# Kernel tuning notes

Measured on AMD Instinct MI355X. Metric: run time of the kernel, lower is better.

Reference implementation:

```python
import math
import jax, jax.numpy as jnp
import numpy as np

T_STEPS = 65536
T_S = 1.0      # net_params['t_s']
THETA = 10.0   # net_params['af_params']['theta']


def _eps_func(mult, tau, epsilon, t_end, t_s):
    vals = []
    for t in np.arange(0, t_end, t_s):
        v = mult * t / tau * math.exp(1 - t / tau)
        if abs(v) < abs(epsilon) and t > tau:
            break
        vals.append(v)
    return vals


def _srm_kernel(mult, tau, epsilon, t_end, t_s):
    # replicates SlayerTrainer._calculate_srm_kernel: pad-to-odd, prepend zeros, flip
    k = _eps_func(mult, tau, epsilon, t_end, t_s)
    if len(k) % 2 == 0:
        k.append(0.0)
    k = np.asarray(k, dtype=np.float32)
    k = np.concatenate([np.zeros(len(k) - 1, np.float32), k])[::-1].copy()
    return k  # (K,), K odd; causal after cross-correlation with pad K//2


def setup_inputs() -> dict:
    key = jax.random.key(0)
    k1, k2, k3 = jax.random.split(key, 3)
    x = jax.random.uniform(k1, (1, 1, 1, 250, T_STEPS), jnp.float32)
    srm = jnp.asarray(_srm_kernel(1.0, 10.0, 1e-4, 200, T_S))                 # sr_params
    ref = jnp.asarray(np.asarray(_eps_func(-20.0, 1.0, 1e-4, 200, T_S), np.float32))  # ref_params
    # SpikeLinear weights, init N(0, std=weights_init)
    w1 = jax.random.normal(k2, (25, 250), jnp.float32) * 4.0
    w2 = jax.random.normal(k3, (1, 25), jnp.float32) * 4.0
    return {"x": x, "srm": srm, "ref": ref, "w1": w1, "w2": w2}


def srm_conv(z, srm):
    # z: (C, T). Per-channel 1-D cross-correlation with 'same' padding,
    # equal to F.conv3d(x, eye-SRM kernel, padding=(0,0,K//2)) * t_s.
    K = srm.shape[0]
    p = K // 2
    lhs = z[:, None, :]            # (C, 1, T) -- channels as batch
    rhs = srm[None, None, :]       # (1, 1, K)
    out = jax.lax.conv_general_dilated(
        lhs, rhs, window_strides=(1,), padding=[(p, p)],
        dimension_numbers=("NCW", "OIW", "NCW"))
    return out[:, 0, :] * T_S


def gen_spikes(pot, ref):
    # Sequential integrate-fire with refractory feedback (slayer_cuda.get_spikes_cuda).
    # pot: (C, T). Carry = per-neuron buffer of scheduled future refractory additions.
    C = pot.shape[0]
    L = ref.shape[0]
    # ref[j] is added to potentials[t+j] on a spike at t (ref[0]==0); after the
    # shift, buf[0] corresponds to time t+1, so schedule ref[1:].
    ref_next = jnp.concatenate([ref[1:], jnp.zeros((1,), pot.dtype)])

    def step(buf, p_t):
        u = p_t + buf[:, 0]                           # membrane incl. refractory
        s = (u >= THETA).astype(pot.dtype)
        buf = jnp.concatenate([buf[:, 1:], jnp.zeros((C, 1), pot.dtype)], axis=1)
        buf = buf + s[:, None] * ref_next[None, :]
        return buf, (u, s / T_S)

    buf0 = jnp.zeros((C, L), pot.dtype)
    _, (u_seq, s_seq) = jax.lax.scan(step, buf0, pot.T)
    return u_seq.T, s_seq.T  # (C, T), (C, T)


def reference(x, srm, ref, w1, w2):
    h = srm_conv(x[0, 0, 0], srm)        # (250, T) SRM-filtered input spikes
    h = w1 @ h                           # (25, T)  SpikeLinear fc1
    _, s1 = gen_spikes(h, ref)           # (25, T)  spikes layer 1
    h = srm_conv(s1, srm)                # (25, T)  SRM on hidden spikes
    h = w2 @ h                           # (1, T)   SpikeLinear fc2
    _, s2 = gen_spikes(h, ref)           # (1, T)
    return s2.reshape(1, 1, 1, 1, -1)
```

## Files before the change

kernel.cpp:

```cpp
#include <hip/hip_runtime.h>


#define T_LEN   65536
#define NCH     250
#define NO1     25
#define KTAPS   129
#define PAD     128
#define SRM_LEN 257
#define REF_LEN 16
#define THETA_F 10.0f
#define LBLK    128
#define NBK     512
#define WARM    128
#define TS      256
#define TT      128
#define FTILE   1024
#define NWORDS  (T_LEN / 32)
#define NGRP    16

__device__ __forceinline__ void srm_step(float p, const float (&rn)[15], float (&b)[15],
                                         unsigned &m, float &sf_out) {
  float u = p + b[0];
  unsigned sp = (u >= THETA_F) ? 1u : 0u;
  float sf = sp ? 1.0f : 0.0f;
#pragma unroll
  for (int j = 0; j < 14; ++j) b[j] = __builtin_fmaf(sf, rn[j], b[j + 1]);
  b[14] = __fmul_rn(sf, rn[14]);
  m = (m << 1) | sp;
  sf_out = sf;
}

__global__ void k_fill(float* out, float v) {
  out[blockIdx.x * 256 + threadIdx.x] = v;
}

__global__ __launch_bounds__(256) void k_prep(const float* __restrict__ w1,
                                              float* __restrict__ w1T) {
  for (int i = threadIdx.x; i < NO1 * NCH; i += 256) {
    int c = i / NO1, o = i - c * NO1;
    w1T[i] = w1[o * NCH + c];
  }
}

__global__ __launch_bounds__(1024, 4) void k_mm1(const float* __restrict__ x,
                                                 const float* __restrict__ w1T,
                                                 float* __restrict__ y1t) {
  __shared__ __align__(16) float part[NGRP][5][TT];
  const int tid = threadIdx.x;
  const int lane = tid & 63;
  const int wv = __builtin_amdgcn_readfirstlane(tid >> 6);
  const int t0 = blockIdx.x * TT;
  const int cs = wv * 15 + (wv < 10 ? wv : 10);
  const int cn = (wv < 10) ? 16 : 15;
  float acc[NO1][2];
#pragma unroll
  for (int o = 0; o < NO1; ++o) { acc[o][0] = 0.f; acc[o][1] = 0.f; }
  const float* xp = x + (size_t)cs * T_LEN + t0 + lane * 2;
  const float* wt = w1T + cs * NO1;
  float2 xb0 = *(const float2*)xp;
  float2 xb1 = *(const float2*)(xp + T_LEN);
  for (int ci = 0; ci < cn; ++ci) {
    float2 xv = xb0;
    xb0 = xb1;
    xb1 = (ci + 2 < cn) ? *(const float2*)(xp + (size_t)(ci + 2) * T_LEN)
                        : make_float2(0.f, 0.f);
    const float* wr = wt + ci * NO1;
#pragma unroll
    for (int o = 0; o < NO1; ++o) {
      float wvv = wr[o];
      acc[o][0] = __builtin_fmaf(wvv, xv.x, acc[o][0]);
      acc[o][1] = __builtin_fmaf(wvv, xv.y, acc[o][1]);
    }
  }
  float* yb = y1t + (size_t)blockIdx.x * (NO1 * TT);
#pragma unroll
  for (int r = 0; r < 5; ++r) {
#pragma unroll
    for (int oo = 0; oo < 5; ++oo) {
      int o = r * 5 + oo;
      *(float2*)&part[wv][oo][lane * 2] = make_float2(acc[o][0], acc[o][1]);
    }
    __syncthreads();
    if (tid < 5 * (TT / 4)) {
      int oo = tid >> 5;
      int p4 = (tid & 31) * 4;
      float4 s = *(const float4*)&part[0][oo][p4];
#pragma unroll
      for (int g = 1; g < NGRP; ++g) {
        float4 p = *(const float4*)&part[g][oo][p4];
        s.x = __fadd_rn(s.x, p.x);
        s.y = __fadd_rn(s.y, p.y);
        s.z = __fadd_rn(s.z, p.z);
        s.w = __fadd_rn(s.w, p.w);
      }
      *(float4*)&yb[(r * 5 + oo) * TT + p4] = s;
    }
    __syncthreads();
  }
}

__global__ __launch_bounds__(256, 8) void k_fir1(const float* __restrict__ y1t,
                                                 const float* __restrict__ srm,
                                                 float* __restrict__ pot1) {
  __shared__ __align__(16) float win[FTILE + PAD];
  const int tid = threadIdx.x;
  const int o = blockIdx.y;
  const int t0 = blockIdx.x * FTILE;
  for (int j = tid; j < FTILE + PAD; j += 256) {
    int g = t0 - PAD + j;
    win[j] = (g >= 0)
        ? y1t[(size_t)(g >> 7) * (NO1 * TT) + o * TT + (g & (TT - 1))] : 0.0f;
  }
  __syncthreads();
  const int base = tid * 4;
  float q0 = 0.0f, q1 = 0.0f, q2 = 0.0f, q3 = 0.0f;
#pragma unroll
  for (int i = 32; i >= 0; --i) {
    float4 v = *(const float4*)&win[base + 4 * i];
#pragma unroll
    for (int l = 3; l >= 0; --l) {
      float vl = (l == 0) ? v.x : (l == 1) ? v.y : (l == 2) ? v.z : v.w;
#pragma unroll
      for (int k = 0; k < 4; ++k) {
        int d = 128 + k - 4 * i - l;
        if (d >= 0 && d <= 128) {
          float e = srm[4 * i + l - k];
          if (k == 0) q0 = __builtin_fmaf(e, vl, q0);
          else if (k == 1) q1 = __builtin_fmaf(e, vl, q1);
          else if (k == 2) q2 = __builtin_fmaf(e, vl, q2);
          else q3 = __builtin_fmaf(e, vl, q3);
        }
      }
    }
  }
  *(float4*)&pot1[(size_t)o * T_LEN + t0 + base] = make_float4(q0, q1, q2, q3);
}

__global__ __launch_bounds__(TS) void k_pot2(const unsigned* __restrict__ s1p,
                                             const float* __restrict__ srm,
                                             const float* __restrict__ w2,
                                             float* __restrict__ pot2) {
  __shared__ float zs[TS + PAD];
  const int tid = threadIdx.x;
  const int t0 = blockIdx.x * TS;
  const int g0 = t0 - PAD;
  {
    int g = g0 + tid;
    float z = 0.0f;
    if (g >= 0) {
      int wi = g >> 5, sh = g & 31;
#pragma unroll
      for (int o = 0; o < NO1; ++o) {
        unsigned wvv = s1p[o * NWORDS + wi];
        z += ((wvv >> sh) & 1u) ? w2[o] : 0.0f;
      }
    }
    zs[tid] = z;
    if (tid < PAD) {
      int g2 = g0 + TS + tid;
      int wi = g2 >> 5, sh = g2 & 31;
      float z2 = 0.0f;
#pragma unroll
      for (int o = 0; o < NO1; ++o) {
        unsigned wvv = s1p[o * NWORDS + wi];
        z2 += ((wvv >> sh) & 1u) ? w2[o] : 0.0f;
      }
      zs[TS + tid] = z2;
    }
  }
  __syncthreads();
  float a = 0.0f;
#pragma unroll
  for (int d = 0; d < KTAPS; ++d) {
    float e = srm[PAD - d];
    a = __builtin_fmaf(e, zs[PAD + tid - d], a);
  }
  pot2[t0 + tid] = a;
}

template <int C, bool PACKED>
__global__ __launch_bounds__(64) void k_scan_spec(const float* __restrict__ pot,
                                                  const float* __restrict__ refk,
                                                  float* __restrict__ s,
                                                  unsigned* __restrict__ sp_,
                                                  unsigned* __restrict__ specin_m,
                                                  unsigned* __restrict__ specout_m,
                                                  float* __restrict__ specout_b) {
  int idx = blockIdx.x * 64 + threadIdx.x;
  if (idx >= C * NBK) return;
  int c = idx / NBK;
  int bb = idx - c * NBK;
  int tsr = bb * LBLK - WARM;
  float rn[15];
#pragma unroll
  for (int j = 0; j < 15; ++j) rn[j] = refk[j + 1];
  float b[15];
#pragma unroll
  for (int j = 0; j < 15; ++j) b[j] = 0.0f;
  unsigned m = 0;
  const float* prow = pot + (size_t)c * T_LEN;
  float* srow = PACKED ? nullptr : (s + (size_t)c * T_LEN);
  unsigned* srowp = PACKED ? (sp_ + (size_t)c * NWORDS) : nullptr;
  for (int k = 0; k < WARM + LBLK; k += 4) {
    if (k == WARM) specin_m[idx] = m & 0x7FFFu;
    int t = tsr + k;
    if (t < 0) continue;
    float4 pv = *(const float4*)(prow + t);
    float s0, s1v, s2, s3;
    srm_step(pv.x, rn, b, m, s0);
    srm_step(pv.y, rn, b, m, s1v);
    srm_step(pv.z, rn, b, m, s2);
    srm_step(pv.w, rn, b, m, s3);
    if (k >= WARM) {
      if (PACKED) {
        if (((t + 3) & 31) == 31) srowp[(t - 28) >> 5] = __brev(m);
      } else {
        *(float4*)(srow + t) = make_float4(s0, s1v, s2, s3);
      }
    }
  }
  specout_m[idx] = m & 0x7FFFu;
#pragma unroll
  for (int j = 0; j < 15; ++j) specout_b[idx * 16 + j] = b[j];
}

template <int C, bool PACKED>
__global__ __launch_bounds__(64) void k_scan_fix(const float* __restrict__ pot,
                                                 const float* __restrict__ refk,
                                                 float* __restrict__ s,
                                                 unsigned* __restrict__ sp_,
                                                 const unsigned* __restrict__ specin_m,
                                                 const unsigned* __restrict__ specout_m,
                                                 const float* __restrict__ specout_b) {
  const int c = blockIdx.x;
  const int lane = threadIdx.x;
  float rn[15];
#pragma unroll
  for (int j = 0; j < 15; ++j) rn[j] = refk[j + 1];
  float b[15];
#pragma unroll
  for (int j = 0; j < 15; ++j) b[j] = 0.0f;
  unsigned m = 0;
  bool haveB = true;
  const float* prow = pot + (size_t)c * T_LEN;
  float* srow = PACKED ? nullptr : (s + (size_t)c * T_LEN);
  unsigned* srowp = PACKED ? (sp_ + (size_t)c * NWORDS) : nullptr;
  unsigned prev_last = 0;

  unsigned siv[NBK / 64], sov[NBK / 64];
#pragma unroll
  for (int g = 0; g < NBK / 64; ++g) {
    siv[g] = specin_m[c * NBK + g * 64 + lane];
    sov[g] = specout_m[c * NBK + g * 64 + lane];
  }
#pragma unroll
  for (int g = 0; g < NBK / 64; ++g) {
    const unsigned si = siv[g];
    const unsigned so = sov[g];
    unsigned so_prev = __shfl_up(so, 1);
    if (lane == 0) so_prev = prev_last;
    const unsigned long long flags = __ballot(si == so_prev);
    prev_last = __shfl(so, 63);
    const unsigned si0 = __shfl(si, 0);
    if (flags == ~0ull && (m & 0x7FFFu) == si0) {
      m = prev_last;
      haveB = false;
      continue;
    }
    for (int r = 0; r < 64; ++r) {
      const unsigned sir = __shfl(si, r);
      const unsigned sor = __shfl(so, r);
      if ((m & 0x7FFFu) == sir) {
        m = sor;
        haveB = false;
      } else {
        const int bbr = g * 64 + r;
        if (!haveB) {
          const int pb = (c * NBK + bbr - 1) * 16;
#pragma unroll
          for (int q2 = 0; q2 < 15; ++q2) b[q2] = specout_b[pb + q2];
          haveB = true;
        }
        const int t0 = bbr * LBLK;
        for (int t = t0; t < t0 + LBLK; t += 4) {
          float4 pv = *(const float4*)(prow + t);
          float s0, s1v, s2, s3;
          srm_step(pv.x, rn, b, m, s0);
          srm_step(pv.y, rn, b, m, s1v);
          srm_step(pv.z, rn, b, m, s2);
          srm_step(pv.w, rn, b, m, s3);
          if (PACKED) {
            if ((((t + 3) & 31) == 31) && lane == 0) srowp[(t - 28) >> 5] = __brev(m);
          } else {
            if (lane == 0) *(float4*)(srow + t) = make_float4(s0, s1v, s2, s3);
          }
        }
        haveB = true;
      }
    }
  }
}

extern "C" void kernel_launch(void* const* d_in, const int* in_sizes, int n_in,
                              void* d_out, int out_size, void* d_ws, size_t ws_size,
                              hipStream_t stream) {
  const float* x    = (const float*)d_in[0];
  const float* srm  = (const float*)d_in[1];
  const float* refk = (const float*)d_in[2];
  const float* w1   = (const float*)d_in[3];
  const float* w2   = (const float*)d_in[4];
  float* out = (float*)d_out;

  float bad = 0.0f;
  if (n_in != 5) bad = 3.0f;
  else if (in_sizes[0] != NCH * T_LEN) bad = 4.0f;
  else if (in_sizes[1] != SRM_LEN)     bad = 5.0f;
  else if (in_sizes[2] != REF_LEN)     bad = 6.0f;
  else if (in_sizes[3] != NO1 * NCH)   bad = 7.0f;
  else if (in_sizes[4] != NO1)         bad = 8.0f;
  else if (out_size != T_LEN)          bad = 9.0f;
  if (bad != 0.0f) {
    k_fill<<<T_LEN / 256, 256, 0, stream>>>(out, bad);
    return;
  }

  size_t off = 0;
  auto alloc = [&](size_t bytes) { size_t o = off; off = (off + bytes + 255) & ~(size_t)255; return o; };
  char* ws = (char*)d_ws;
  size_t oY1  = alloc((size_t)NO1 * T_LEN * 4);
  size_t oP1  = alloc((size_t)NO1 * T_LEN * 4);
  size_t oS1P = alloc((size_t)NO1 * NWORDS * 4);
  size_t oP2  = alloc((size_t)T_LEN * 4);
  size_t oW1T = alloc((size_t)NO1 * NCH * 4);
  if (ws_size < off) {
    k_fill<<<T_LEN / 256, 256, 0, stream>>>(out, 2.0f);
    return;
  }

  float*    y1t  = (float*)(ws + oY1);
  float*    pot1 = (float*)(ws + oP1);
  unsigned* s1p  = (unsigned*)(ws + oS1P);
  float*    pot2 = (float*)(ws + oP2);
  float*    w1T  = (float*)(ws + oW1T);
  char* yb = ws + oY1;
  unsigned* si1 = (unsigned*)(yb);
  unsigned* so1 = (unsigned*)(yb + 51200);
  float*    sb1 = (float*)   (yb + 102400);
  unsigned* si2 = (unsigned*)(yb + 921600);
  unsigned* so2 = (unsigned*)(yb + 923648);
  float*    sb2 = (float*)   (yb + 925696);

  k_prep<<<1, 256, 0, stream>>>(w1, w1T);
  k_mm1<<<T_LEN / TT, 1024, 0, stream>>>(x, w1T, y1t);
  k_fir1<<<dim3(T_LEN / FTILE, NO1), 256, 0, stream>>>(y1t, srm, pot1);
  k_scan_spec<NO1, true><<<(NO1 * NBK + 63) / 64, 64, 0, stream>>>(
      pot1, refk, nullptr, s1p, si1, so1, sb1);
  k_scan_fix<NO1, true><<<NO1, 64, 0, stream>>>(pot1, refk, nullptr, s1p, si1, so1, sb1);
  k_pot2<<<T_LEN / TS, TS, 0, stream>>>(s1p, srm, w2, pot2);
  k_scan_spec<1, false><<<(NBK + 63) / 64, 64, 0, stream>>>(
      pot2, refk, out, nullptr, si2, so2, sb2);
  k_scan_fix<1, false><<<1, 64, 0, stream>>>(pot2, refk, out, nullptr, si2, so2, sb2);
}
```

Before: 100.0 us.

## Drop weight transpose kernel, deepen load prefetch, register-block pot2 FIR, batch scan loads

Removes the k_prep launch so k_mm1 reads w1 directly with wave-uniform indexing. The k_mm1 channel loop now prefetches x rows four at a time in a double-buffered scheme instead of two. k_pot2 processes 1024-sample tiles with each thread producing four outputs from float4 shared-memory reads, matching the fir1 scheme and cutting redundant halo work and LDS reads. The spec scan loads 16 potentials per iteration to expose more memory-level parallelism, at the cost of more register pressure.

```diff
diff --git a/kernel.cpp b/kernel.cpp
--- a/kernel.cpp
+++ b/kernel.cpp
@@ -12,9 +12,9 @@
 #define LBLK    128
 #define NBK     512
 #define WARM    128
-#define TS      256
 #define TT      128
 #define FTILE   1024
+#define FT2     1024
 #define NWORDS  (T_LEN / 32)
 #define NGRP    16
 
@@ -34,16 +34,8 @@
   out[blockIdx.x * 256 + threadIdx.x] = v;
 }
 
-__global__ __launch_bounds__(256) void k_prep(const float* __restrict__ w1,
-                                              float* __restrict__ w1T) {
-  for (int i = threadIdx.x; i < NO1 * NCH; i += 256) {
-    int c = i / NO1, o = i - c * NO1;
-    w1T[i] = w1[o * NCH + c];
-  }
-}
-
 __global__ __launch_bounds__(1024, 4) void k_mm1(const float* __restrict__ x,
-                                                 const float* __restrict__ w1T,
+                                                 const float* __restrict__ w1,
                                                  float* __restrict__ y1t) {
   __shared__ __align__(16) float part[NGRP][5][TT];
   const int tid = threadIdx.x;
@@ -56,21 +48,29 @@
 #pragma unroll
   for (int o = 0; o < NO1; ++o) { acc[o][0] = 0.f; acc[o][1] = 0.f; }
   const float* xp = x + (size_t)cs * T_LEN + t0 + lane * 2;
-  const float* wt = w1T + cs * NO1;
-  float2 xb0 = *(const float2*)xp;
-  float2 xb1 = *(const float2*)(xp + T_LEN);
-  for (int ci = 0; ci < cn; ++ci) {
-    float2 xv = xb0;
-    xb0 = xb1;
-    xb1 = (ci + 2 < cn) ? *(const float2*)(xp + (size_t)(ci + 2) * T_LEN)
-                        : make_float2(0.f, 0.f);
-    const float* wr = wt + ci * NO1;
-#pragma unroll
-    for (int o = 0; o < NO1; ++o) {
-      float wvv = wr[o];
-      acc[o][0] = __builtin_fmaf(wvv, xv.x, acc[o][0]);
-      acc[o][1] = __builtin_fmaf(wvv, xv.y, acc[o][1]);
-    }
+
+  auto ld = [&](int ci) -> float2 {
+    return (ci < cn) ? *(const float2*)(xp + (size_t)ci * T_LEN)
+                     : make_float2(0.f, 0.f);
+  };
+  auto use = [&](int ci, float2 xv) {
+    if (ci < cn) {
+#pragma unroll
+      for (int o = 0; o < NO1; ++o) {
+        float wvv = w1[o * NCH + cs + ci];
+        acc[o][0] = __builtin_fmaf(wvv, xv.x, acc[o][0]);
+        acc[o][1] = __builtin_fmaf(wvv, xv.y, acc[o][1]);
+      }
+    }
+  };
+
+  float2 A0 = ld(0), A1 = ld(1), A2 = ld(2), A3 = ld(3);
+  float2 B0, B1, B2, B3;
+  for (int cb = 0; cb < cn; cb += 8) {
+    B0 = ld(cb + 4); B1 = ld(cb + 5); B2 = ld(cb + 6); B3 = ld(cb + 7);
+    use(cb + 0, A0); use(cb + 1, A1); use(cb + 2, A2); use(cb + 3, A3);
+    A0 = ld(cb + 8); A1 = ld(cb + 9); A2 = ld(cb + 10); A3 = ld(cb + 11);
+    use(cb + 4, B0); use(cb + 5, B1); use(cb + 6, B2); use(cb + 7, B3);
   }
   float* yb = y1t + (size_t)blockIdx.x * (NO1 * TT);
 #pragma unroll
@@ -136,16 +136,15 @@
   *(float4*)&pot1[(size_t)o * T_LEN + t0 + base] = make_float4(q0, q1, q2, q3);
 }
 
-__global__ __launch_bounds__(TS) void k_pot2(const unsigned* __restrict__ s1p,
-                                             const float* __restrict__ srm,
-                                             const float* __restrict__ w2,
-                                             float* __restrict__ pot2) {
-  __shared__ float zs[TS + PAD];
+__global__ __launch_bounds__(256) void k_pot2(const unsigned* __restrict__ s1p,
+                                              const float* __restrict__ srm,
+                                              const float* __restrict__ w2,
+                                              float* __restrict__ pot2) {
+  __shared__ __align__(16) float zs[FT2 + PAD];
   const int tid = threadIdx.x;
-  const int t0 = blockIdx.x * TS;
-  const int g0 = t0 - PAD;
-  {
-    int g = g0 + tid;
+  const int t0 = blockIdx.x * FT2;
+  for (int j = tid; j < FT2 + PAD; j += 256) {
+    int g = t0 - PAD + j;
     float z = 0.0f;
     if (g >= 0) {
       int wi = g >> 5, sh = g & 31;
@@ -155,27 +154,31 @@
         z += ((wvv >> sh) & 1u) ? w2[o] : 0.0f;
       }
     }
-    zs[tid] = z;
-    if (tid < PAD) {
-      int g2 = g0 + TS + tid;
-      int wi = g2 >> 5, sh = g2 & 31;
-      float z2 = 0.0f;
-#pragma unroll
-      for (int o = 0; o < NO1; ++o) {
-        unsigned wvv = s1p[o * NWORDS + wi];
-        z2 += ((wvv >> sh) & 1u) ? w2[o] : 0.0f;
-      }
-      zs[TS + tid] = z2;
-    }
+    zs[j] = z;
   }
   __syncthreads();
-  float a = 0.0f;
-#pragma unroll
-  for (int d = 0; d < KTAPS; ++d) {
-    float e = srm[PAD - d];
-    a = __builtin_fmaf(e, zs[PAD + tid - d], a);
-  }
-  pot2[t0 + tid] = a;
+  const int base = tid * 4;
+  float q0 = 0.0f, q1 = 0.0f, q2 = 0.0f, q3 = 0.0f;
+#pragma unroll
+  for (int i = 32; i >= 0; --i) {
+    float4 v = *(const float4*)&zs[base + 4 * i];
+#pragma unroll
+    for (int l = 3; l >= 0; --l) {
+      float vl = (l == 0) ? v.x : (l == 1) ? v.y : (l == 2) ? v.z : v.w;
+#pragma unroll
+      for (int k = 0; k < 4; ++k) {
+        int d = 128 + k - 4 * i - l;
+        if (d >= 0 && d <= 128) {
+          float e = srm[4 * i + l - k];
+          if (k == 0) q0 = __builtin_fmaf(e, vl, q0);
+          else if (k == 1) q1 = __builtin_fmaf(e, vl, q1);
+          else if (k == 2) q2 = __builtin_fmaf(e, vl, q2);
+          else q3 = __builtin_fmaf(e, vl, q3);
+        }
+      }
+    }
+  }
+  *(float4*)&pot2[t0 + base] = make_float4(q0, q1, q2, q3);
 }
 
 template <int C, bool PACKED>
@@ -201,23 +204,35 @@
   const float* prow = pot + (size_t)c * T_LEN;
   float* srow = PACKED ? nullptr : (s + (size_t)c * T_LEN);
   unsigned* srowp = PACKED ? (sp_ + (size_t)c * NWORDS) : nullptr;
-  for (int k = 0; k < WARM + LBLK; k += 4) {
-    if (k == WARM) specin_m[idx] = m & 0x7FFFu;
-    int t = tsr + k;
-    if (t < 0) continue;
-    float4 pv = *(const float4*)(prow + t);
+
+  auto proc4 = [&](float4 pv, int tg, bool emit) {
     float s0, s1v, s2, s3;
     srm_step(pv.x, rn, b, m, s0);
     srm_step(pv.y, rn, b, m, s1v);
     srm_step(pv.z, rn, b, m, s2);
     srm_step(pv.w, rn, b, m, s3);
-    if (k >= WARM) {
+    if (emit) {
       if (PACKED) {
-        if (((t + 3) & 31) == 31) srowp[(t - 28) >> 5] = __brev(m);
+        if (((tg + 3) & 31) == 31) srowp[(tg - 28) >> 5] = __brev(m);
       } else {
-        *(float4*)(srow + t) = make_float4(s0, s1v, s2, s3);
-      }
-    }
+        *(float4*)(srow + tg) = make_float4(s0, s1v, s2, s3);
+      }
+    }
+  };
+
+  for (int k = 0; k < WARM + LBLK; k += 16) {
+    if (k == WARM) specin_m[idx] = m & 0x7FFFu;
+    int t = tsr + k;
+    if (t < 0) continue;
+    float4 p0 = *(const float4*)(prow + t);
+    float4 p1 = *(const float4*)(prow + t + 4);
+    float4 p2 = *(const float4*)(prow + t + 8);
+    float4 p3 = *(const float4*)(prow + t + 12);
+    const bool emit = (k >= WARM);
+    proc4(p0, t, emit);
+    proc4(p1, t + 4, emit);
+    proc4(p2, t + 8, emit);
+    proc4(p3, t + 12, emit);
   }
   specout_m[idx] = m & 0x7FFFu;
 #pragma unroll
@@ -331,7 +346,6 @@
   size_t oP1  = alloc((size_t)NO1 * T_LEN * 4);
   size_t oS1P = alloc((size_t)NO1 * NWORDS * 4);
   size_t oP2  = alloc((size_t)T_LEN * 4);
-  size_t oW1T = alloc((size_t)NO1 * NCH * 4);
   if (ws_size < off) {
     k_fill<<<T_LEN / 256, 256, 0, stream>>>(out, 2.0f);
     return;
@@ -341,7 +355,6 @@
   float*    pot1 = (float*)(ws + oP1);
   unsigned* s1p  = (unsigned*)(ws + oS1P);
   float*    pot2 = (float*)(ws + oP2);
-  float*    w1T  = (float*)(ws + oW1T);
   char* yb = ws + oY1;
   unsigned* si1 = (unsigned*)(yb);
   unsigned* so1 = (unsigned*)(yb + 51200);
@@ -350,13 +363,12 @@
   unsigned* so2 = (unsigned*)(yb + 923648);
   float*    sb2 = (float*)   (yb + 925696);
 
-  k_prep<<<1, 256, 0, stream>>>(w1, w1T);
-  k_mm1<<<T_LEN / TT, 1024, 0, stream>>>(x, w1T, y1t);
+  k_mm1<<<T_LEN / TT, 1024, 0, stream>>>(x, w1, y1t);
   k_fir1<<<dim3(T_LEN / FTILE, NO1), 256, 0, stream>>>(y1t, srm, pot1);
   k_scan_spec<NO1, true><<<(NO1 * NBK + 63) / 64, 64, 0, stream>>>(
       pot1, refk, nullptr, s1p, si1, so1, sb1);
   k_scan_fix<NO1, true><<<NO1, 64, 0, stream>>>(pot1, refk, nullptr, s1p, si1, so1, sb1);
-  k_pot2<<<T_LEN / TS, TS, 0, stream>>>(s1p, srm, w2, pot2);
+  k_pot2<<<T_LEN / FT2, 256, 0, stream>>>(s1p, srm, w2, pot2);
   k_scan_spec<1, false><<<(NBK + 63) / 64, 64, 0, stream>>>(
       pot2, refk, out, nullptr, si2, so2, sb2);
   k_scan_fix<1, false><<<1, 64, 0, stream>>>(pot2, refk, out, nullptr, si2, so2, sb2);
```

Measured after the change: 98.65 us. About the same (-1.4%).
